# Kernel optimization log

Hardware: AMD Instinct MI355X
Metric: run time of the kernel (lower is better)

## Reference

```python
import jax, jax.numpy as jnp
import numpy as np

T, B, D_IN, E, HA, HB, D_OUT = 64, 64, 4096, 128, 128, 128, 4096


def setup_inputs() -> dict:
    key = jax.random.key(0)
    ks = jax.random.split(key, 18)

    def u(k, shape, fan):
        b = 1.0 / np.sqrt(fan)
        return jax.random.uniform(k, shape, jnp.float32, -b, b)

    return {
        "x": jax.random.uniform(ks[0], (T, B, D_IN), jnp.float32),
        "W_emb": u(ks[1], (E, D_IN), D_IN), "b_emb": u(ks[2], (E,), D_IN),
        "W_ih_a": u(ks[3], (3 * HA, E), HA), "W_hh_a": u(ks[4], (3 * HA, HA), HA),
        "b_ih_a": u(ks[5], (3 * HA,), HA), "b_hh_a": u(ks[6], (3 * HA,), HA),
        "W_ih_b": u(ks[7], (3 * HB, E), HB), "W_hh_b": u(ks[8], (3 * HB, HB), HB),
        "b_ih_b": u(ks[9], (3 * HB,), HB), "b_hh_b": u(ks[10], (3 * HB,), HB),
        "w_alpha": u(ks[11], (1, HA), HA), "b_alpha": u(ks[12], (1,), HA),
        "W_beta": u(ks[13], (E, HB), HB), "b_beta": u(ks[14], (E,), HB),
        "W_out": u(ks[15], (D_OUT, E), E), "b_out": u(ks[16], (D_OUT,), E),
    }


def _gru_states(emb, W_ih, W_hh, b_ih, b_hh):
    # For every query position i, run a GRU over the reversed prefix
    # emb[i], emb[i-1], ..., emb[0] from h0 = 0. All T queries are batched.
    # Returns hs[s, i, b, h] = hidden of query i after step s (input emb[i-s]).
    Tlen, Bsz, _ = emb.shape
    H = W_hh.shape[1]
    i_arr = jnp.arange(Tlen)

    def step(h, s):
        idx = jnp.clip(i_arr - s, 0, Tlen - 1)          # (T,) input index per query
        xs = emb[idx]                                    # (T, B, E)
        gi = xs @ W_ih.T + b_ih                          # (T, B, 3H)
        gh = h @ W_hh.T + b_hh
        i_r, i_z, i_n = jnp.split(gi, 3, axis=-1)
        h_r, h_z, h_n = jnp.split(gh, 3, axis=-1)
        r = jax.nn.sigmoid(i_r + h_r)
        z = jax.nn.sigmoid(i_z + h_z)
        n = jnp.tanh(i_n + r * h_n)
        h_new = (1.0 - z) * n + z * h
        return h_new, h_new

    h0 = jnp.zeros((Tlen, Bsz, H), emb.dtype)
    _, hs = jax.lax.scan(step, h0, jnp.arange(Tlen))
    return hs  # (S, T, B, H)


def _retain_forward(x, W_emb, b_emb, W_ih_a, W_hh_a, b_ih_a, b_hh_a,
                    W_ih_b, W_hh_b, b_ih_b, b_hh_b, w_alpha, b_alpha,
                    W_beta, b_beta, W_out, b_out):
    Tlen = x.shape[0]
    emb = x @ W_emb.T + b_emb                            # (T, B, E)

    hs_a = _gru_states(emb, W_ih_a, W_hh_a, b_ih_a, b_hh_a)  # (S, T, B, HA)
    hs_b = _gru_states(emb, W_ih_b, W_hh_b, b_ih_b, b_hh_b)  # (S, T, B, HB)

    i_arr = jnp.arange(Tlen)
    # reverse_h[i, j] = hidden after processing emb[i..j] (reverse order) = hs[i - j, i]
    rev = jnp.clip(i_arr[:, None] - i_arr[None, :], 0, Tlen - 1)  # (T, T)
    rh_a = hs_a[rev, i_arr[:, None]] * 0.5               # (T, T, B, HA)
    rh_b = hs_b[rev, i_arr[:, None]] * 0.5               # (T, T, B, HB)

    mask = (i_arr[None, :] <= i_arr[:, None])            # (T, T): j <= i valid
    logits = jnp.einsum('ijbh,h->ijb', rh_a, w_alpha[0]) + b_alpha[0]
    logits = jnp.where(mask[:, :, None], logits, -1e9)
    alpha = jax.nn.softmax(logits, axis=1)               # softmax over prefix steps j
    alpha = alpha * mask[:, :, None].astype(alpha.dtype)

    beta = jnp.tanh(rh_b @ W_beta.T + b_beta)            # (T, T, B, E)

    # c[i] = mean_{j<=i} alpha[i,j] * beta[i,j] * emb[j]
    c = jnp.einsum('ijb,ijbe->ibe', alpha, beta * emb[None, :, :, :])
    counts = jnp.arange(1, Tlen + 1, dtype=c.dtype)[:, None, None]
    c = c / counts

    return jax.nn.sigmoid(c @ W_out.T + b_out)           # (T, B, D_OUT)


def reference(x, W_emb, b_emb, W_ih_a, W_hh_a, b_ih_a, b_hh_a,
              W_ih_b, W_hh_b, b_ih_b, b_hh_b, w_alpha, b_alpha,
              W_beta, b_beta, W_out, b_out):
    return _retain_forward(x, W_emb, b_emb, W_ih_a, W_hh_a, b_ih_a, b_hh_a,
                           W_ih_b, W_hh_b, b_ih_b, b_hh_b, w_alpha, b_alpha,
                           W_beta, b_beta, W_out, b_out)
```

## Files before the change

### kernel.cpp

```cpp
#include <hip/hip_runtime.h>
#include <hip/hip_bf16.h>


typedef __attribute__((ext_vector_type(8))) short short8;
typedef __attribute__((ext_vector_type(4))) float f32x4;
typedef _Float16 half8 __attribute__((ext_vector_type(8)));

#define MFMA16(a, b, c) __builtin_amdgcn_mfma_f32_16x16x32_bf16((a), (b), (c), 0, 0, 0)

#define LOG2E 1.4426950408889634f
#define TLOG2E 2.8853900817779268f

__device__ __forceinline__ unsigned pkbf(float a, float b) {
  __hip_bfloat162 t = __float22bfloat162_rn(float2{a, b});
  return *reinterpret_cast<unsigned*>(&t);
}
__device__ __forceinline__ float ex2(float x) { return __builtin_amdgcn_exp2f(x); }
__device__ __forceinline__ float rcpa(float x) { return __builtin_amdgcn_rcpf(x); }
__device__ __forceinline__ float tanh2(float y) {
  float e = ex2(-fmaxf(y, -126.0f));
  return (1.0f - e) * rcpa(1.0f + e);
}

#define OFF_PART   0u
#define OFF_GI3    16777216u
#define OFF_EMBBF  25165824u
#define OFF_CBF    26214400u
#define OFF_WEMB   27262976u
#define OFF_WOUT   28311552u
#define OFF_WHHA   29360128u
#define OFF_WHHB   29458432u
#define OFF_WIH    29556736u
#define OFF_WBETA  29753344u

__global__ void k_prep(const float* W_emb, const float* W_out,
                       const float* W_hh_a, const float* W_hh_b,
                       const float* W_ih_a, const float* W_ih_b,
                       const float* W_beta,
                       unsigned* wemb, unsigned* wout,
                       unsigned* whha, unsigned* whhb,
                       unsigned* wih, unsigned* wbeta) {
  const unsigned total = 630784u;
  for (unsigned idx = blockIdx.x * 256u + threadIdx.x; idx < total;
       idx += gridDim.x * 256u) {
    unsigned i = idx;
    if (i < 262144u) { float2 v = ((const float2*)W_emb)[i]; wemb[i] = pkbf(v.x, v.y); continue; }
    i -= 262144u;
    if (i < 262144u) { float2 v = ((const float2*)W_out)[i]; wout[i] = pkbf(v.x, v.y); continue; }
    i -= 262144u;
    if (i < 24576u) {
      float2 v = ((const float2*)W_hh_a)[i];
      const float sc = ((i >> 13) == 2u) ? TLOG2E : LOG2E;
      whha[i] = pkbf(sc * v.x, sc * v.y); continue;
    }
    i -= 24576u;
    if (i < 24576u) {
      float2 v = ((const float2*)W_hh_b)[i];
      const float sc = ((i >> 13) == 2u) ? TLOG2E : LOG2E;
      whhb[i] = pkbf(sc * v.x, sc * v.y); continue;
    }
    i -= 24576u;
    if (i < 24576u) {
      float2 v = ((const float2*)W_ih_a)[i];
      const float sc = ((i >> 13) == 2u) ? TLOG2E : LOG2E;
      wih[i] = pkbf(sc * v.x, sc * v.y); continue;
    }
    i -= 24576u;
    if (i < 24576u) {
      float2 v = ((const float2*)W_ih_b)[i];
      const float sc = ((i >> 13) == 2u) ? TLOG2E : LOG2E;
      wih[24576u + i] = pkbf(sc * v.x, sc * v.y); continue;
    }
    i -= 24576u;
    { float2 v = ((const float2*)W_beta)[i]; wbeta[i] = pkbf(LOG2E * v.x, LOG2E * v.y); }
  }
}

__global__ __launch_bounds__(256) void k_emb_gemm(const float* __restrict__ x,
                                                  const unsigned short* __restrict__ wemb,
                                                  float* __restrict__ part) {
  const int mt = blockIdx.x >> 3, kc = blockIdx.x & 7;
  const int w = threadIdx.x >> 6, lane = threadIdx.x & 63, q = lane >> 4, ln = lane & 15;
  const f32x4 zero = {0.f, 0.f, 0.f, 0.f};
  f32x4 acc[8];
#pragma unroll
  for (int b = 0; b < 8; ++b) acc[b] = zero;

  const float* xA = x + (size_t)(mt * 64 + w * 16 + ln) * 4096 + kc * 512 + q * 8;

  for (int kk = 0; kk < 16; ++kk) {
    const int ko = kk * 32;
    float4 u0 = *(const float4*)(xA + ko);
    float4 u1 = *(const float4*)(xA + ko + 4);
    union { short8 v; unsigned u[4]; } a0;
    a0.u[0] = pkbf(u0.x, u0.y); a0.u[1] = pkbf(u0.z, u0.w);
    a0.u[2] = pkbf(u1.x, u1.y); a0.u[3] = pkbf(u1.z, u1.w);
#pragma unroll
    for (int nt = 0; nt < 8; ++nt) {
      short8 b = *(const short8*)(wemb + (size_t)(nt * 16 + ln) * 4096 + kc * 512 + ko + q * 8);
      acc[nt] = MFMA16(a0.v, b, acc[nt]);
    }
  }
  const int mbase = mt * 64 + w * 16 + q * 4;
#pragma unroll
  for (int nt = 0; nt < 8; ++nt)
#pragma unroll
    for (int r = 0; r < 4; ++r)
      part[(size_t)kc * 524288 + (size_t)(mbase + r) * 128 + nt * 16 + ln] = acc[nt][r];
}

__global__ void k_emb_reduce(const float* __restrict__ part, const float* __restrict__ b_emb,
                             _Float16* __restrict__ gih, unsigned* __restrict__ embbf) {
  const unsigned pidx = blockIdx.x * 256u + threadIdx.x;
  const unsigned e0 = (pidx * 2u) & 127u;
  const unsigned m = pidx >> 6;
  float2 s = ((const float2*)b_emb)[e0 >> 1];
#pragma unroll
  for (int kc = 0; kc < 8; ++kc) {
    float2 v = ((const float2*)(part + (size_t)kc * 524288u))[pidx];
    s.x += v.x; s.y += v.y;
  }
  gih[(size_t)m * 1024u + e0 * 8u + 6u] = (_Float16)s.x;
  gih[(size_t)m * 1024u + (e0 + 1u) * 8u + 6u] = (_Float16)s.y;
  embbf[pidx] = pkbf(s.x, s.y);
}

__global__ __launch_bounds__(256) void k_gi_gemm(const unsigned short* __restrict__ embbf,
                                                 const unsigned short* __restrict__ wih,
                                                 const float* __restrict__ b_ih_a,
                                                 const float* __restrict__ b_ih_b,
                                                 const float* __restrict__ b_hh_a,
                                                 const float* __restrict__ b_hh_b,
                                                 _Float16* __restrict__ gih) {
  const int mt = blockIdx.x / 6, nt6 = blockIdx.x % 6, nbase = nt6 * 128;
  const int w = threadIdx.x >> 6, lane = threadIdx.x & 63, q = lane >> 4, ln = lane & 15;
  const f32x4 zero = {0.f, 0.f, 0.f, 0.f};
  f32x4 acc[2][8];
#pragma unroll
  for (int a = 0; a < 2; ++a)
#pragma unroll
    for (int b = 0; b < 8; ++b) acc[a][b] = zero;

#pragma unroll
  for (int kk = 0; kk < 4; ++kk) {
    const int ko = kk * 32 + q * 8;
    short8 a0 = *(const short8*)(embbf + (size_t)(mt * 128 + (2 * w) * 16 + ln) * 128 + ko);
    short8 a1 = *(const short8*)(embbf + (size_t)(mt * 128 + (2 * w + 1) * 16 + ln) * 128 + ko);
#pragma unroll
    for (int nt = 0; nt < 8; ++nt) {
      short8 b = *(const short8*)(wih + (size_t)(nbase + nt * 16 + ln) * 128 + ko);
      acc[0][nt] = MFMA16(a0, b, acc[0][nt]);
      acc[1][nt] = MFMA16(a1, b, acc[1][nt]);
    }
  }
#pragma unroll
  for (int nt = 0; nt < 8; ++nt) {
    const int g = nbase + nt * 16 + ln;
    const int gg = g >> 7, kout = g & 127;
    float bias;
    if (g < 384) bias = b_ih_a[g] + ((gg < 2) ? b_hh_a[g] : 0.0f);
    else {
      const int g2 = g - 384;
      bias = b_ih_b[g2] + ((gg < 5) ? b_hh_b[g2] : 0.0f);
    }
    bias *= (gg == 2 || gg == 5) ? TLOG2E : LOG2E;
#pragma unroll
    for (int st = 0; st < 2; ++st) {
      const int mbase = mt * 128 + (2 * w + st) * 16 + q * 4;
#pragma unroll
      for (int r = 0; r < 4; ++r)
        gih[(size_t)(mbase + r) * 1024 + kout * 8 + gg] = (_Float16)(acc[st][nt][r] + bias);
    }
  }
}

__global__ __launch_bounds__(512) __attribute__((amdgpu_waves_per_eu(2, 2)))
void k_recur(const _Float16* __restrict__ gih,
             const unsigned short* __restrict__ whha, const unsigned short* __restrict__ whhb,
             const unsigned short* __restrict__ wbeta,
             const float* __restrict__ b_hh_a, const float* __restrict__ b_hh_b,
             const float* __restrict__ b_beta, const float* __restrict__ b_alpha,
             const float* __restrict__ w_alpha,
             unsigned short* __restrict__ cbf) {
  const int tid = threadIdx.x, w = tid >> 6, lane = tid & 63, q = lane >> 4, ln = lane & 15;
  const int p = blockIdx.x >> 3, btile = blockIdx.x & 7;
  const int i1 = p, i2 = 63 - p;
  const int kout = w * 16 + ln;

  __shared__ unsigned short hA[2][16 * 136], hB[2][16 * 136];

  for (int idx = tid; idx < 16 * 136; idx += 512) { hA[0][idx] = 0; hB[0][idx] = 0; }

  const int iq = (q < 2) ? i1 : i2;
  const _Float16* gp[4];
#pragma unroll
  for (int r = 0; r < 4; ++r) {
    const int b = btile * 8 + (q & 1) * 4 + r;
    gp[r] = gih + (size_t)(iq * 64 + b) * 1024 + kout * 8;
  }

  short8 fra[3][4], frb[3][4];
#pragma unroll
  for (int g = 0; g < 3; ++g) {
    const unsigned short* ba = whha + (size_t)(g * 128 + kout) * 128;
    const unsigned short* bb = whhb + (size_t)(g * 128 + kout) * 128;
#pragma unroll
    for (int kc = 0; kc < 4; ++kc) {
      fra[g][kc] = *(const short8*)(ba + kc * 32 + q * 8);
      frb[g][kc] = *(const short8*)(bb + kc * 32 + q * 8);
    }
  }
#pragma unroll
  for (int g = 0; g < 3; ++g)
#pragma unroll
    for (int kc = 0; kc < 4; ++kc) {
      asm volatile("" : "+a"(fra[g][kc]));
      asm volatile("" : "+a"(frb[g][kc]));
    }

  short8 fbe[4];
#pragma unroll
  for (int kc = 0; kc < 4; ++kc) {
    fbe[kc] = *(const short8*)(wbeta + (size_t)(w * 16 + ln) * 128 + kc * 32 + q * 8);
    asm volatile("" : "+a"(fbe[kc]));
  }

  short8 fal[4];
#pragma unroll
  for (int kc = 0; kc < 4; ++kc) {
    float4 w0 = *(const float4*)(w_alpha + kc * 32 + q * 8);
    float4 w1 = *(const float4*)(w_alpha + kc * 32 + q * 8 + 4);
    union { short8 v; unsigned u[4]; } t;
    t.u[0] = pkbf(0.5f * LOG2E * w0.x, 0.5f * LOG2E * w0.y);
    t.u[1] = pkbf(0.5f * LOG2E * w0.z, 0.5f * LOG2E * w0.w);
    t.u[2] = pkbf(0.5f * LOG2E * w1.x, 0.5f * LOG2E * w1.y);
    t.u[3] = pkbf(0.5f * LOG2E * w1.z, 0.5f * LOG2E * w1.w);
    const short8 z8 = {0, 0, 0, 0, 0, 0, 0, 0};
    fal[kc] = (ln == 0) ? t.v : z8;
    asm volatile("" : "+a"(fal[kc]));
  }

  const float bhnA = TLOG2E * b_hh_a[256 + kout];
  const float bhnB = TLOG2E * b_hh_b[256 + kout];
  const float bbet = TLOG2E * b_beta[kout];
  const float bal = LOG2E * b_alpha[0];

  float hRA[4], hRB[4], cac[4], lreg[4], embp[4];
#pragma unroll
  for (int r = 0; r < 4; ++r) { hRA[r] = 0.f; hRB[r] = 0.f; cac[r] = 0.f; lreg[r] = 0.f; embp[r] = 0.f; }

  const f32x4 zero = {0.f, 0.f, 0.f, 0.f};
  int jj = iq;
  half8 ngv[4];
#pragma unroll
  for (int r = 0; r < 4; ++r) ngv[r] = *(const half8*)gp[r];

  __syncthreads();

  for (int s = 0; s <= i2; ++s) {
    const int rb = s & 1, wb = rb ^ 1;

    half8 gv[4];
#pragma unroll
    for (int r = 0; r < 4; ++r) gv[r] = ngv[r];

    short8 haf[4], hbf[4];
#pragma unroll
    for (int kc = 0; kc < 4; ++kc) {
      haf[kc] = *(const short8*)(hA[rb] + ln * 136 + kc * 32 + q * 8);
      hbf[kc] = *(const short8*)(hB[rb] + ln * 136 + kc * 32 + q * 8);
    }

    f32x4 accA[3] = {zero, zero, zero}, accB[3] = {zero, zero, zero};
    f32x4 accV = zero, accL = zero;
#pragma unroll
    for (int kc = 0; kc < 4; ++kc) {
#pragma unroll
      for (int g = 0; g < 3; ++g) {
        accA[g] = MFMA16(haf[kc], fra[g][kc], accA[g]);
        accB[g] = MFMA16(hbf[kc], frb[g][kc], accB[g]);
      }
      accV = MFMA16(hbf[kc], fbe[kc], accV);
      accL = MFMA16(haf[kc], fal[kc], accL);
    }

    const bool act = ((unsigned)(s - 1) <= (unsigned)iq);
#pragma unroll
    for (int r = 0; r < 4; ++r) {
      const float logit =
          __int_as_float(__builtin_amdgcn_ds_swizzle(__float_as_int(accL[r]), 16)) + bal;
      const float pp = act ? ex2(logit) : 0.0f;
      lreg[r] += pp;
      const float beta = tanh2(accV[r] + bbet);
      cac[r] += pp * beta * embp[r];
    }

#pragma unroll
    for (int r = 0; r < 4; ++r) {
      const int rowoff = (q * 4 + r) * 136 + kout;

      const float erA = ex2(-((float)gv[r][0] + accA[0][r]));
      const float rA = rcpa(1.0f + erA);
      const float tA = (float)gv[r][2] + rA * (accA[2][r] + bhnA);
      const float enA = ex2(-fmaxf(tA, -62.0f));
      const float ezA = ex2(-fmaxf((float)gv[r][1] + accA[1][r], -62.0f));
      const float apnA = 1.0f + enA, apzA = 1.0f + ezA;
      const float numA = fmaf(hRA[r], apnA, ezA * (1.0f - enA));
      const float hnA = numA * rcpa(apnA * apzA);
      hRA[r] = hnA;
      hA[wb][rowoff] = (unsigned short)pkbf(hnA, hnA);

      const float erB = ex2(-((float)gv[r][3] + accB[0][r]));
      const float rB = rcpa(1.0f + erB);
      const float tB = (float)gv[r][5] + rB * (accB[2][r] + bhnB);
      const float enB = ex2(-fmaxf(tB, -62.0f));
      const float ezB = ex2(-fmaxf((float)gv[r][4] + accB[1][r], -62.0f));
      const float apnB = 1.0f + enB, apzB = 1.0f + ezB;
      const float numB = fmaf(hRB[r], apnB, ezB * (1.0f - enB));
      const float hnB = numB * rcpa(apnB * apzB);
      hRB[r] = hnB;
      hB[wb][rowoff] = (unsigned short)pkbf(hnB, hnB);

      embp[r] = (float)gv[r][6];
    }

    if (jj > 0) {
      --jj;
#pragma unroll
      for (int r = 0; r < 4; ++r) gp[r] -= 65536;
    }
#pragma unroll
    for (int r = 0; r < 4; ++r) ngv[r] = *(const half8*)gp[r];

    asm volatile("s_waitcnt lgkmcnt(0)\n\ts_barrier" ::: "memory");
  }

  {
    const int rb2 = (i2 + 1) & 1;
    short8 haf[4], hbf[4];
#pragma unroll
    for (int kc = 0; kc < 4; ++kc) {
      haf[kc] = *(const short8*)(hA[rb2] + ln * 136 + kc * 32 + q * 8);
      hbf[kc] = *(const short8*)(hB[rb2] + ln * 136 + kc * 32 + q * 8);
    }
    f32x4 accV = zero, accL = zero;
#pragma unroll
    for (int kc = 0; kc < 4; ++kc) {
      accV = MFMA16(hbf[kc], fbe[kc], accV);
      accL = MFMA16(haf[kc], fal[kc], accL);
    }
    const bool act = (iq == i2);
#pragma unroll
    for (int r = 0; r < 4; ++r) {
      const float logit =
          __int_as_float(__builtin_amdgcn_ds_swizzle(__float_as_int(accL[r]), 16)) + bal;
      const float pp = act ? ex2(logit) : 0.0f;
      lreg[r] += pp;
      const float beta = tanh2(accV[r] + bbet);
      cac[r] += pp * beta * embp[r];
    }
  }

#pragma unroll
  for (int r = 0; r < 4; ++r) {
    const int b = btile * 8 + (q & 1) * 4 + r;
    const float val = cac[r] * rcpa(lreg[r] * (float)(iq + 1));
    cbf[(size_t)(iq * 64 + b) * 128 + kout] = (unsigned short)pkbf(val, val);
  }
}

__global__ __launch_bounds__(256) void k_out_gemm(const unsigned short* __restrict__ cbf,
                                                  const unsigned short* __restrict__ wout,
                                                  const float* __restrict__ b_out,
                                                  float* __restrict__ out) {
  const int mt = blockIdx.x >> 7, ntb = blockIdx.x & 127, nbase = ntb * 32;
  const int w = threadIdx.x >> 6, lane = threadIdx.x & 63, q = lane >> 4, ln = lane & 15;
  const f32x4 zero = {0.f, 0.f, 0.f, 0.f};
  f32x4 acc[2][2] = {{zero, zero}, {zero, zero}};

#pragma unroll
  for (int kk = 0; kk < 4; ++kk) {
    const int ko = kk * 32 + q * 8;
    short8 a0 = *(const short8*)(wout + (size_t)(nbase + ln) * 128 + ko);
    short8 a1 = *(const short8*)(wout + (size_t)(nbase + 16 + ln) * 128 + ko);
    short8 b0 = *(const short8*)(cbf + (size_t)(mt * 128 + (w * 2 + 0) * 16 + ln) * 128 + ko);
    short8 b1 = *(const short8*)(cbf + (size_t)(mt * 128 + (w * 2 + 1) * 16 + ln) * 128 + ko);
    acc[0][0] = MFMA16(a0, b0, acc[0][0]);
    acc[0][1] = MFMA16(a0, b1, acc[0][1]);
    acc[1][0] = MFMA16(a1, b0, acc[1][0]);
    acc[1][1] = MFMA16(a1, b1, acc[1][1]);
  }
#pragma unroll
  for (int st = 0; st < 2; ++st) {
    const int n0 = nbase + st * 16 + q * 4;
    const float4 bo = *(const float4*)(b_out + n0);
#pragma unroll
    for (int j = 0; j < 2; ++j) {
      const int m = mt * 128 + (w * 2 + j) * 16 + ln;
      float4 o;
      o.x = rcpa(1.0f + ex2(-LOG2E * (acc[st][j][0] + bo.x)));
      o.y = rcpa(1.0f + ex2(-LOG2E * (acc[st][j][1] + bo.y)));
      o.z = rcpa(1.0f + ex2(-LOG2E * (acc[st][j][2] + bo.z)));
      o.w = rcpa(1.0f + ex2(-LOG2E * (acc[st][j][3] + bo.w)));
      *(float4*)(out + (size_t)m * 4096 + n0) = o;
    }
  }
}

extern "C" void kernel_launch(void* const* d_in, const int* in_sizes, int n_in,
                              void* d_out, int out_size, void* d_ws, size_t ws_size,
                              hipStream_t stream) {
  const float* x      = (const float*)d_in[0];
  const float* W_emb  = (const float*)d_in[1];
  const float* b_emb  = (const float*)d_in[2];
  const float* W_ih_a = (const float*)d_in[3];
  const float* W_hh_a = (const float*)d_in[4];
  const float* b_ih_a = (const float*)d_in[5];
  const float* b_hh_a = (const float*)d_in[6];
  const float* W_ih_b = (const float*)d_in[7];
  const float* W_hh_b = (const float*)d_in[8];
  const float* b_ih_b = (const float*)d_in[9];
  const float* b_hh_b = (const float*)d_in[10];
  const float* w_alpha = (const float*)d_in[11];
  const float* b_alpha = (const float*)d_in[12];
  const float* W_beta = (const float*)d_in[13];
  const float* b_beta = (const float*)d_in[14];
  const float* W_out  = (const float*)d_in[15];
  const float* b_out  = (const float*)d_in[16];
  float* out = (float*)d_out;

  char* ws = (char*)d_ws;
  float*          part   = (float*)(ws + OFF_PART);
  _Float16*       gih    = (_Float16*)(ws + OFF_GI3);
  unsigned*       embbf  = (unsigned*)(ws + OFF_EMBBF);
  unsigned short* cbf    = (unsigned short*)(ws + OFF_CBF);
  unsigned*       wemb   = (unsigned*)(ws + OFF_WEMB);
  unsigned*       wout   = (unsigned*)(ws + OFF_WOUT);
  unsigned*       whha   = (unsigned*)(ws + OFF_WHHA);
  unsigned*       whhb   = (unsigned*)(ws + OFF_WHHB);
  unsigned*       wih    = (unsigned*)(ws + OFF_WIH);
  unsigned*       wbeta  = (unsigned*)(ws + OFF_WBETA);

  k_prep<<<1024, 256, 0, stream>>>(W_emb, W_out, W_hh_a, W_hh_b, W_ih_a, W_ih_b,
                                   W_beta, wemb, wout, whha, whhb, wih, wbeta);
  k_emb_gemm<<<512, 256, 0, stream>>>(x, (const unsigned short*)wemb, part);
  k_emb_reduce<<<1024, 256, 0, stream>>>(part, b_emb, gih, embbf);
  k_gi_gemm<<<192, 256, 0, stream>>>((const unsigned short*)embbf, (const unsigned short*)wih,
                                     b_ih_a, b_ih_b, b_hh_a, b_hh_b, gih);
  k_recur<<<256, 512, 0, stream>>>(gih, (const unsigned short*)whha,
                                   (const unsigned short*)whhb, (const unsigned short*)wbeta,
                                   b_hh_a, b_hh_b, b_beta, b_alpha, w_alpha, cbf);
  k_out_gemm<<<4096, 256, 0, stream>>>(cbf, (const unsigned short*)wout, b_out, out);
}
```

Baseline: 344.8 us.

## Fuse output GEMM and sigmoid into recurrence kernel epilogue

```diff
diff --git a/kernel.cpp b/kernel.cpp
--- a/kernel.cpp
+++ b/kernel.cpp
@@ -181,7 +181,9 @@
              const float* __restrict__ b_hh_a, const float* __restrict__ b_hh_b,
              const float* __restrict__ b_beta, const float* __restrict__ b_alpha,
              const float* __restrict__ w_alpha,
-             unsigned short* __restrict__ cbf) {
+             const unsigned short* __restrict__ wout,
+             const float* __restrict__ b_out,
+             float* __restrict__ out) {
   const int tid = threadIdx.x, w = tid >> 6, lane = tid & 63, q = lane >> 4, ln = lane & 15;
   const int p = blockIdx.x >> 3, btile = blockIdx.x & 7;
   const int i1 = p, i2 = 63 - p;
@@ -235,8 +237,7 @@
     t.u[1] = pkbf(0.5f * LOG2E * w0.z, 0.5f * LOG2E * w0.w);
     t.u[2] = pkbf(0.5f * LOG2E * w1.x, 0.5f * LOG2E * w1.y);
     t.u[3] = pkbf(0.5f * LOG2E * w1.z, 0.5f * LOG2E * w1.w);
-    const short8 z8 = {0, 0, 0, 0, 0, 0, 0, 0};
-    fal[kc] = (ln == 0) ? t.v : z8;
+    fal[kc] = t.v;
     asm volatile("" : "+a"(fal[kc]));
   }
 
@@ -287,8 +288,7 @@
     const bool act = ((unsigned)(s - 1) <= (unsigned)iq);
 #pragma unroll
     for (int r = 0; r < 4; ++r) {
-      const float logit =
-          __int_as_float(__builtin_amdgcn_ds_swizzle(__float_as_int(accL[r]), 16)) + bal;
+      const float logit = accL[r] + bal;
       const float pp = act ? ex2(logit) : 0.0f;
       lreg[r] += pp;
       const float beta = tanh2(accV[r] + bbet);
@@ -352,8 +352,7 @@
     const bool act = (iq == i2);
 #pragma unroll
     for (int r = 0; r < 4; ++r) {
-      const float logit =
-          __int_as_float(__builtin_amdgcn_ds_swizzle(__float_as_int(accL[r]), 16)) + bal;
+      const float logit = accL[r] + bal;
       const float pp = act ? ex2(logit) : 0.0f;
       lreg[r] += pp;
       const float beta = tanh2(accV[r] + bbet);
@@ -361,48 +360,43 @@
     }
   }
 
-#pragma unroll
-  for (int r = 0; r < 4; ++r) {
-    const int b = btile * 8 + (q & 1) * 4 + r;
-    const float val = cac[r] * rcpa(lreg[r] * (float)(iq + 1));
-    cbf[(size_t)(iq * 64 + b) * 128 + kout] = (unsigned short)pkbf(val, val);
-  }
-}
-
-__global__ __launch_bounds__(256) void k_out_gemm(const unsigned short* __restrict__ cbf,
-                                                  const unsigned short* __restrict__ wout,
-                                                  const float* __restrict__ b_out,
-                                                  float* __restrict__ out) {
-  const int mt = blockIdx.x >> 7, ntb = blockIdx.x & 127, nbase = ntb * 32;
-  const int w = threadIdx.x >> 6, lane = threadIdx.x & 63, q = lane >> 4, ln = lane & 15;
-  const f32x4 zero = {0.f, 0.f, 0.f, 0.f};
-  f32x4 acc[2][2] = {{zero, zero}, {zero, zero}};
-
-#pragma unroll
-  for (int kk = 0; kk < 4; ++kk) {
-    const int ko = kk * 32 + q * 8;
-    short8 a0 = *(const short8*)(wout + (size_t)(nbase + ln) * 128 + ko);
-    short8 a1 = *(const short8*)(wout + (size_t)(nbase + 16 + ln) * 128 + ko);
-    short8 b0 = *(const short8*)(cbf + (size_t)(mt * 128 + (w * 2 + 0) * 16 + ln) * 128 + ko);
-    short8 b1 = *(const short8*)(cbf + (size_t)(mt * 128 + (w * 2 + 1) * 16 + ln) * 128 + ko);
-    acc[0][0] = MFMA16(a0, b0, acc[0][0]);
-    acc[0][1] = MFMA16(a0, b1, acc[0][1]);
-    acc[1][0] = MFMA16(a1, b0, acc[1][0]);
-    acc[1][1] = MFMA16(a1, b1, acc[1][1]);
-  }
-#pragma unroll
-  for (int st = 0; st < 2; ++st) {
-    const int n0 = nbase + st * 16 + q * 4;
-    const float4 bo = *(const float4*)(b_out + n0);
-#pragma unroll
-    for (int j = 0; j < 2; ++j) {
-      const int m = mt * 128 + (w * 2 + j) * 16 + ln;
+  __syncthreads();
+  {
+    const int crow0 = (q >= 2 ? 8 : 0) + (q & 1) * 4;
+#pragma unroll
+    for (int r = 0; r < 4; ++r) {
+      const float val = cac[r] * rcpa(lreg[r] * (float)(iq + 1));
+      hA[0][(crow0 + r) * 136 + kout] = (unsigned short)pkbf(val, val);
+    }
+  }
+  __syncthreads();
+
+  {
+    short8 cb[4];
+#pragma unroll
+    for (int kc = 0; kc < 4; ++kc)
+      cb[kc] = *(const short8*)(hA[0] + ln * 136 + kc * 32 + q * 8);
+
+    const int m_glob = ((ln >= 8) ? i2 : i1) * 64 + btile * 8 + (ln & 7);
+    float* orow = out + (size_t)m_glob * 4096;
+    const int nb0 = w * 512;
+
+    for (int nt = 0; nt < 32; ++nt) {
+      const int n16 = nb0 + nt * 16;
+      f32x4 acc = zero;
+#pragma unroll
+      for (int kc = 0; kc < 4; ++kc) {
+        short8 a = *(const short8*)(wout + (size_t)(n16 + ln) * 128 + kc * 32 + q * 8);
+        acc = MFMA16(a, cb[kc], acc);
+      }
+      const int n0 = n16 + q * 4;
+      const float4 bo = *(const float4*)(b_out + n0);
       float4 o;
-      o.x = rcpa(1.0f + ex2(-LOG2E * (acc[st][j][0] + bo.x)));
-      o.y = rcpa(1.0f + ex2(-LOG2E * (acc[st][j][1] + bo.y)));
-      o.z = rcpa(1.0f + ex2(-LOG2E * (acc[st][j][2] + bo.z)));
-      o.w = rcpa(1.0f + ex2(-LOG2E * (acc[st][j][3] + bo.w)));
-      *(float4*)(out + (size_t)m * 4096 + n0) = o;
+      o.x = rcpa(1.0f + ex2(-LOG2E * (acc[0] + bo.x)));
+      o.y = rcpa(1.0f + ex2(-LOG2E * (acc[1] + bo.y)));
+      o.z = rcpa(1.0f + ex2(-LOG2E * (acc[2] + bo.z)));
+      o.w = rcpa(1.0f + ex2(-LOG2E * (acc[3] + bo.w)));
+      *(float4*)(orow + n0) = o;
     }
   }
 }
@@ -433,7 +427,6 @@
   float*          part   = (float*)(ws + OFF_PART);
   _Float16*       gih    = (_Float16*)(ws + OFF_GI3);
   unsigned*       embbf  = (unsigned*)(ws + OFF_EMBBF);
-  unsigned short* cbf    = (unsigned short*)(ws + OFF_CBF);
   unsigned*       wemb   = (unsigned*)(ws + OFF_WEMB);
   unsigned*       wout   = (unsigned*)(ws + OFF_WOUT);
   unsigned*       whha   = (unsigned*)(ws + OFF_WHHA);
@@ -449,6 +442,6 @@
                                      b_ih_a, b_ih_b, b_hh_a, b_hh_b, gih);
   k_recur<<<256, 512, 0, stream>>>(gih, (const unsigned short*)whha,
                                    (const unsigned short*)whhb, (const unsigned short*)wbeta,
-                                   b_hh_a, b_hh_b, b_beta, b_alpha, w_alpha, cbf);
-  k_out_gemm<<<4096, 256, 0, stream>>>(cbf, (const unsigned short*)wout, b_out, out);
-}
+                                   b_hh_a, b_hh_b, b_beta, b_alpha, w_alpha,
+                                   (const unsigned short*)wout, b_out, out);
+}
```

Result: no change. 340.4 us (-1.3%).
